# Optimization experiments

Hardware: AMD Instinct MI355X
Metric: run time of the kernel (lower is better)

## Reference

```python
import jax, jax.numpy as jnp
import numpy as np
import math

N_STATIONS = 50  # N in [N, 7, 56] causal matrix


def setup_inputs() -> dict:
    key = jax.random.key(0)
    k1, k2, k3, k4 = jax.random.split(key, 4)
    B, L, H, E = 3200, 7, 8, 64
    S, D = 56, 64
    queries = jax.random.normal(k1, (B, L, H, E), dtype=jnp.float32)
    keys = jax.random.normal(k2, (B, S, H, E), dtype=jnp.float32)
    values = jax.random.normal(k3, (B, S, H, D), dtype=jnp.float32)
    # station-specific multiplicative causal matrix in [0, 1]
    attn_mask = jax.random.uniform(k4, (N_STATIONS, L, S), dtype=jnp.float32)
    return {"queries": queries, "keys": keys, "values": values, "attn_mask": attn_mask}


def reference(queries, keys, values, attn_mask):
    B, L, H, E = queries.shape
    S = values.shape[1]
    N = attn_mask.shape[0]  # number of stations; B % N == 0
    ab = B // N  # actual batch size per station group
    scale = 1.0 / math.sqrt(E)
    # raw scores [B, H, L, S]
    scores = jnp.einsum('blhe,bshe->bhls', queries, keys)
    # multiplicative station-specific mask: reshape batch into (ab, N) and
    # broadcast mask [N, L, S] over (ab, H)
    masked = scores.reshape(ab, N, H, L, S) * attn_mask[None, :, None, :, :]
    masked = masked.reshape(B, H, L, S)
    # note: scale is applied AFTER masking, as in the original module
    A = jax.nn.softmax(scale * masked, axis=-1)  # dropout is identity at eval
    V = jnp.einsum('bhls,bshd->blhd', A, values)
    return V
```

## Files before the change

kernel.cpp:

```cpp
#include <hip/hip_runtime.h>
#include <math.h>


typedef __attribute__((ext_vector_type(8))) _Float16 half8;

#define GLDS(gp, lp) __builtin_amdgcn_global_load_lds(                        \
    (const __attribute__((address_space(1))) void*)(gp),                      \
    (__attribute__((address_space(3))) void*)(lp), 16, 0, 0)

__launch_bounds__(64, 4)
__global__ void fullattn_kernel(const float* __restrict__ q,
                                const float* __restrict__ k,
                                const float* __restrict__ v,
                                const float* __restrict__ mask,
                                float* __restrict__ out,
                                int nstations) {
    __shared__ __align__(16) float    KL[56 * 64];
    __shared__ __align__(16) float    VL[56 * 64];
    __shared__ __align__(16) _Float16 QL[7 * 64];

    const int lane = threadIdx.x;
    const int unit = blockIdx.x;
    const int b    = unit >> 3;
    const int h    = unit & 7;
    const int st   = b % nstations;

    const int kbase = b * 28672 + h * 64;
    const int qbase = b * 3584  + h * 64;

    {
        const int r = (lane >> 4);
        const int p = lane & 15;
#pragma unroll
        for (int j = 0; j < 14; ++j) {
            const int row = j * 4 + r;
            const int c   = p ^ (row & 15);
            GLDS(k + kbase + row * 512 + c * 4, (char*)KL + j * 1024);
        }
    }
    __builtin_amdgcn_sched_barrier(0);

    float qr[7];
#pragma unroll
    for (int l = 0; l < 7; ++l) qr[l] = q[qbase + l * 512 + lane];
    __builtin_amdgcn_sched_barrier(0);

    const int ml = (lane < 56) ? lane : 55;
    float m[7];
#pragma unroll
    for (int l = 0; l < 7; ++l)
        m[l] = mask[st * 392 + l * 56 + ml] * 0.125f;
    __builtin_amdgcn_sched_barrier(0);

    {
        const int r = (lane >> 4);
        const int p = lane & 15;
#pragma unroll
        for (int j = 0; j < 14; ++j) {
            const int row = j * 4 + r;
            GLDS(v + kbase + row * 512 + p * 4, (char*)VL + j * 1024);
        }
    }
    __builtin_amdgcn_sched_barrier(0);

    asm volatile("s_waitcnt vmcnt(28)" ::: "memory");
    __builtin_amdgcn_sched_barrier(0);

#pragma unroll
    for (int l = 0; l < 7; ++l) QL[l * 64 + lane] = (_Float16)qr[l];

    const int x16 = ml & 15;
    float acc[7];
#pragma unroll
    for (int l = 0; l < 7; ++l) acc[l] = 0.0f;

#pragma unroll
    for (int c2 = 0; c2 < 8; ++c2) {
        const float4 kv0 = *(const float4*)(&KL[ml * 64 + (((2 * c2)     ^ x16) << 2)]);
        const float4 kv1 = *(const float4*)(&KL[ml * 64 + (((2 * c2 + 1) ^ x16) << 2)]);
#pragma unroll
        for (int l = 0; l < 7; ++l) {
            const half8 qv = *(const half8*)(&QL[l * 64 + c2 * 8]);
            acc[l] = fmaf(kv0.x, (float)qv[0], acc[l]);
            acc[l] = fmaf(kv0.y, (float)qv[1], acc[l]);
            acc[l] = fmaf(kv0.z, (float)qv[2], acc[l]);
            acc[l] = fmaf(kv0.w, (float)qv[3], acc[l]);
            acc[l] = fmaf(kv1.x, (float)qv[4], acc[l]);
            acc[l] = fmaf(kv1.y, (float)qv[5], acc[l]);
            acc[l] = fmaf(kv1.z, (float)qv[6], acc[l]);
            acc[l] = fmaf(kv1.w, (float)qv[7], acc[l]);
        }
    }

    float* pbuf = (float*)KL;
    float rdenom[7];
#pragma unroll
    for (int l = 0; l < 7; ++l) {
        const float sc = acc[l] * m[l];
        const float p  = (lane < 56) ? __expf(sc) : 0.0f;
        float sum = p;
#pragma unroll
        for (int off = 32; off >= 1; off >>= 1)
            sum += __shfl_xor(sum, off);
        pbuf[l * 64 + lane] = p;
        rdenom[l] = __builtin_amdgcn_rcpf(sum);
    }

    asm volatile("s_waitcnt vmcnt(0)" ::: "memory");
    __builtin_amdgcn_sched_barrier(0);

    float facc[7];
#pragma unroll
    for (int l = 0; l < 7; ++l) facc[l] = 0.0f;

#pragma unroll
    for (int s4 = 0; s4 < 14; ++s4) {
        const float vv0 = VL[(s4 * 4 + 0) * 64 + lane];
        const float vv1 = VL[(s4 * 4 + 1) * 64 + lane];
        const float vv2 = VL[(s4 * 4 + 2) * 64 + lane];
        const float vv3 = VL[(s4 * 4 + 3) * 64 + lane];
#pragma unroll
        for (int l = 0; l < 7; ++l) {
            const float4 p4 = *(const float4*)(&pbuf[l * 64 + s4 * 4]);
            facc[l] = fmaf(p4.x, vv0, facc[l]);
            facc[l] = fmaf(p4.y, vv1, facc[l]);
            facc[l] = fmaf(p4.z, vv2, facc[l]);
            facc[l] = fmaf(p4.w, vv3, facc[l]);
        }
    }

#pragma unroll
    for (int l = 0; l < 7; ++l)
        out[qbase + l * 512 + lane] = facc[l] * rdenom[l];
}

extern "C" void kernel_launch(void* const* d_in, const int* in_sizes, int n_in,
                              void* d_out, int out_size, void* d_ws, size_t ws_size,
                              hipStream_t stream) {
    const float* q    = (const float*)d_in[0];
    const float* k    = (const float*)d_in[1];
    const float* v    = (const float*)d_in[2];
    const float* mask = (const float*)d_in[3];
    float* out        = (float*)d_out;

    const int B = in_sizes[0] / (7 * 8 * 64);
    const int nstations = in_sizes[3] / (7 * 56);

    fullattn_kernel<<<dim3(B * 8), dim3(64), 0, stream>>>(q, k, v, mask, out, nstations);
}
```

Before: 160.6 us.

## Convert to persistent kernel with double-buffered K/V prefetch across units

Replaces the one-block-per-(batch, head) launch with 512 persistent single-wave blocks. Each block loops over a contiguous range of units and double-buffers K/V in LDS. While one unit computes, the next unit's K/V (async global-to-LDS) and its Q and mask values are already being fetched, with hand-tuned vmcnt waits between stages. This aims to hide load latency and block launch overhead, but it lowers resident waves per CU and relies on exact vmcnt accounting.

```diff
diff --git a/kernel.cpp b/kernel.cpp
--- a/kernel.cpp
+++ b/kernel.cpp
@@ -8,130 +8,154 @@
     (const __attribute__((address_space(1))) void*)(gp),                      \
     (__attribute__((address_space(3))) void*)(lp), 16, 0, 0)
 
-__launch_bounds__(64, 4)
+__launch_bounds__(64, 1)
 __global__ void fullattn_kernel(const float* __restrict__ q,
                                 const float* __restrict__ k,
                                 const float* __restrict__ v,
                                 const float* __restrict__ mask,
                                 float* __restrict__ out,
-                                int nstations) {
-    __shared__ __align__(16) float    KL[56 * 64];
-    __shared__ __align__(16) float    VL[56 * 64];
+                                int nstations, int nunits, int nblocks) {
+    __shared__ __align__(16) float K0[56 * 64];
+    __shared__ __align__(16) float K1[56 * 64];
+    __shared__ __align__(16) float V0[56 * 64];
+    __shared__ __align__(16) float V1[56 * 64];
     __shared__ __align__(16) _Float16 QL[7 * 64];
 
     const int lane = threadIdx.x;
-    const int unit = blockIdx.x;
-    const int b    = unit >> 3;
-    const int h    = unit & 7;
-    const int st   = b % nstations;
+    const int bid  = blockIdx.x;
+    const int ustart = (int)(((long long)bid * nunits) / nblocks);
+    const int uend   = (int)(((long long)(bid + 1) * nunits) / nblocks);
+    if (ustart >= uend) return;
 
-    const int kbase = b * 28672 + h * 64;
-    const int qbase = b * 3584  + h * 64;
+    const int ml = (lane < 56) ? lane : 55;
+    const int rr = lane >> 4;
+    const int pp = lane & 15;
 
-    {
-        const int r = (lane >> 4);
-        const int p = lane & 15;
+    float qr_a[7], m_a[7], qr_b[7], m_b[7];
+
+    auto issue_kv = [&](int u, float* KB, float* VB) {
+        const int kbase = (u >> 3) * 28672 + (u & 7) * 64;
 #pragma unroll
         for (int j = 0; j < 14; ++j) {
-            const int row = j * 4 + r;
-            const int c   = p ^ (row & 15);
-            GLDS(k + kbase + row * 512 + c * 4, (char*)KL + j * 1024);
+            const int row = j * 4 + rr;
+            const int c   = pp ^ (row & 15);
+            GLDS(k + kbase + row * 512 + c * 4, (char*)KB + j * 1024);
         }
-    }
-    __builtin_amdgcn_sched_barrier(0);
-
-    float qr[7];
-#pragma unroll
-    for (int l = 0; l < 7; ++l) qr[l] = q[qbase + l * 512 + lane];
-    __builtin_amdgcn_sched_barrier(0);
-
-    const int ml = (lane < 56) ? lane : 55;
-    float m[7];
-#pragma unroll
-    for (int l = 0; l < 7; ++l)
-        m[l] = mask[st * 392 + l * 56 + ml] * 0.125f;
-    __builtin_amdgcn_sched_barrier(0);
-
-    {
-        const int r = (lane >> 4);
-        const int p = lane & 15;
 #pragma unroll
         for (int j = 0; j < 14; ++j) {
-            const int row = j * 4 + r;
-            GLDS(v + kbase + row * 512 + p * 4, (char*)VL + j * 1024);
+            const int row = j * 4 + rr;
+            GLDS(v + kbase + row * 512 + pp * 4, (char*)VB + j * 1024);
         }
-    }
-    __builtin_amdgcn_sched_barrier(0);
+    };
+    auto load_qm = [&](int u, float (&qr)[7], float (&m)[7]) {
+        const int qbase = (u >> 3) * 3584 + (u & 7) * 64;
+#pragma unroll
+        for (int l = 0; l < 7; ++l) qr[l] = q[qbase + l * 512 + lane];
+        const int st = (u >> 3) % nstations;
+#pragma unroll
+        for (int l = 0; l < 7; ++l)
+            m[l] = mask[st * 392 + l * 56 + ml] * 0.125f;
+    };
+    auto compute = [&](int u, float* KB, float* VB,
+                       const float (&qr)[7], const float (&m)[7]) {
+#pragma unroll
+        for (int l = 0; l < 7; ++l) QL[l * 64 + lane] = (_Float16)qr[l];
 
-    asm volatile("s_waitcnt vmcnt(28)" ::: "memory");
-    __builtin_amdgcn_sched_barrier(0);
+        const int x16 = ml & 15;
+        float acc[7];
+#pragma unroll
+        for (int l = 0; l < 7; ++l) acc[l] = 0.0f;
 
 #pragma unroll
-    for (int l = 0; l < 7; ++l) QL[l * 64 + lane] = (_Float16)qr[l];
+        for (int c2 = 0; c2 < 8; ++c2) {
+            const float4 kv0 = *(const float4*)(&KB[ml * 64 + (((2 * c2)     ^ x16) << 2)]);
+            const float4 kv1 = *(const float4*)(&KB[ml * 64 + (((2 * c2 + 1) ^ x16) << 2)]);
+#pragma unroll
+            for (int l = 0; l < 7; ++l) {
+                const half8 qv = *(const half8*)(&QL[l * 64 + c2 * 8]);
+                acc[l] = fmaf(kv0.x, (float)qv[0], acc[l]);
+                acc[l] = fmaf(kv0.y, (float)qv[1], acc[l]);
+                acc[l] = fmaf(kv0.z, (float)qv[2], acc[l]);
+                acc[l] = fmaf(kv0.w, (float)qv[3], acc[l]);
+                acc[l] = fmaf(kv1.x, (float)qv[4], acc[l]);
+                acc[l] = fmaf(kv1.y, (float)qv[5], acc[l]);
+                acc[l] = fmaf(kv1.z, (float)qv[6], acc[l]);
+                acc[l] = fmaf(kv1.w, (float)qv[7], acc[l]);
+            }
+        }
 
-    const int x16 = ml & 15;
-    float acc[7];
-#pragma unroll
-    for (int l = 0; l < 7; ++l) acc[l] = 0.0f;
-
-#pragma unroll
-    for (int c2 = 0; c2 < 8; ++c2) {
-        const float4 kv0 = *(const float4*)(&KL[ml * 64 + (((2 * c2)     ^ x16) << 2)]);
-        const float4 kv1 = *(const float4*)(&KL[ml * 64 + (((2 * c2 + 1) ^ x16) << 2)]);
+        float* pbuf = KB;
+        float rdenom[7];
 #pragma unroll
         for (int l = 0; l < 7; ++l) {
-            const half8 qv = *(const half8*)(&QL[l * 64 + c2 * 8]);
-            acc[l] = fmaf(kv0.x, (float)qv[0], acc[l]);
-            acc[l] = fmaf(kv0.y, (float)qv[1], acc[l]);
-            acc[l] = fmaf(kv0.z, (float)qv[2], acc[l]);
-            acc[l] = fmaf(kv0.w, (float)qv[3], acc[l]);
-            acc[l] = fmaf(kv1.x, (float)qv[4], acc[l]);
-            acc[l] = fmaf(kv1.y, (float)qv[5], acc[l]);
-            acc[l] = fmaf(kv1.z, (float)qv[6], acc[l]);
-            acc[l] = fmaf(kv1.w, (float)qv[7], acc[l]);
+            const float sc = acc[l] * m[l];
+            const float p  = (lane < 56) ? __expf(sc) : 0.0f;
+            float sum = p;
+#pragma unroll
+            for (int off = 32; off >= 1; off >>= 1)
+                sum += __shfl_xor(sum, off);
+            pbuf[l * 64 + lane] = p;
+            rdenom[l] = __builtin_amdgcn_rcpf(sum);
         }
+
+        float facc[7];
+#pragma unroll
+        for (int l = 0; l < 7; ++l) facc[l] = 0.0f;
+#pragma unroll
+        for (int s4 = 0; s4 < 14; ++s4) {
+            const float vv0 = VB[(s4 * 4 + 0) * 64 + lane];
+            const float vv1 = VB[(s4 * 4 + 1) * 64 + lane];
+            const float vv2 = VB[(s4 * 4 + 2) * 64 + lane];
+            const float vv3 = VB[(s4 * 4 + 3) * 64 + lane];
+#pragma unroll
+            for (int l = 0; l < 7; ++l) {
+                const float4 p4 = *(const float4*)(&pbuf[l * 64 + s4 * 4]);
+                facc[l] = fmaf(p4.x, vv0, facc[l]);
+                facc[l] = fmaf(p4.y, vv1, facc[l]);
+                facc[l] = fmaf(p4.z, vv2, facc[l]);
+                facc[l] = fmaf(p4.w, vv3, facc[l]);
+            }
+        }
+
+        const int qbase = (u >> 3) * 3584 + (u & 7) * 64;
+#pragma unroll
+        for (int l = 0; l < 7; ++l)
+            out[qbase + l * 512 + lane] = facc[l] * rdenom[l];
+    };
+
+    auto main_iter = [&](int u, float* KR, float* VR, float* KW, float* VW,
+                         const float (&qc)[7], const float (&mc)[7],
+                         float (&qn)[7], float (&mn)[7]) {
+        issue_kv(u + 1, KW, VW);
+        load_qm(u + 1, qn, mn);
+        __builtin_amdgcn_sched_barrier(0);
+        asm volatile("s_waitcnt vmcnt(49)" ::: "memory");
+        __builtin_amdgcn_sched_barrier(0);
+        compute(u, KR, VR, qc, mc);
+    };
+    auto last_iter = [&](int u, float* KR, float* VR,
+                         const float (&qc)[7], const float (&mc)[7]) {
+        __builtin_amdgcn_sched_barrier(0);
+        asm volatile("s_waitcnt vmcnt(7)" ::: "memory");
+        __builtin_amdgcn_sched_barrier(0);
+        compute(u, KR, VR, qc, mc);
+    };
+
+    issue_kv(ustart, K0, V0);
+    load_qm(ustart, qr_a, m_a);
+
+    int u = ustart;
+    while (u + 2 < uend) {
+        main_iter(u,     K0, V0, K1, V1, qr_a, m_a, qr_b, m_b);
+        main_iter(u + 1, K1, V1, K0, V0, qr_b, m_b, qr_a, m_a);
+        u += 2;
     }
-
-    float* pbuf = (float*)KL;
-    float rdenom[7];
-#pragma unroll
-    for (int l = 0; l < 7; ++l) {
-        const float sc = acc[l] * m[l];
-        const float p  = (lane < 56) ? __expf(sc) : 0.0f;
-        float sum = p;
-#pragma unroll
-        for (int off = 32; off >= 1; off >>= 1)
-            sum += __shfl_xor(sum, off);
-        pbuf[l * 64 + lane] = p;
-        rdenom[l] = __builtin_amdgcn_rcpf(sum);
+    if (u + 1 < uend) {
+        main_iter(u, K0, V0, K1, V1, qr_a, m_a, qr_b, m_b);
+        last_iter(u + 1, K1, V1, qr_b, m_b);
+    } else {
+        last_iter(u, K0, V0, qr_a, m_a);
     }
-
-    asm volatile("s_waitcnt vmcnt(0)" ::: "memory");
-    __builtin_amdgcn_sched_barrier(0);
-
-    float facc[7];
-#pragma unroll
-    for (int l = 0; l < 7; ++l) facc[l] = 0.0f;
-
-#pragma unroll
-    for (int s4 = 0; s4 < 14; ++s4) {
-        const float vv0 = VL[(s4 * 4 + 0) * 64 + lane];
-        const float vv1 = VL[(s4 * 4 + 1) * 64 + lane];
-        const float vv2 = VL[(s4 * 4 + 2) * 64 + lane];
-        const float vv3 = VL[(s4 * 4 + 3) * 64 + lane];
-#pragma unroll
-        for (int l = 0; l < 7; ++l) {
-            const float4 p4 = *(const float4*)(&pbuf[l * 64 + s4 * 4]);
-            facc[l] = fmaf(p4.x, vv0, facc[l]);
-            facc[l] = fmaf(p4.y, vv1, facc[l]);
-            facc[l] = fmaf(p4.z, vv2, facc[l]);
-            facc[l] = fmaf(p4.w, vv3, facc[l]);
-        }
-    }
-
-#pragma unroll
-    for (int l = 0; l < 7; ++l)
-        out[qbase + l * 512 + lane] = facc[l] * rdenom[l];
 }
 
 extern "C" void kernel_launch(void* const* d_in, const int* in_sizes, int n_in,
@@ -145,6 +169,9 @@
 
     const int B = in_sizes[0] / (7 * 8 * 64);
     const int nstations = in_sizes[3] / (7 * 56);
+    const int nunits = B * 8;
+    const int nblocks = 512;
 
-    fullattn_kernel<<<dim3(B * 8), dim3(64), 0, stream>>>(q, k, v, mask, out, nstations);
+    fullattn_kernel<<<dim3(nblocks), dim3(64), 0, stream>>>(q, k, v, mask, out,
+                                                            nstations, nunits, nblocks);
 }
```

Measured after the change: 262.2 us. 63.3% more time.

## Use MFMA f16 matrix instructions for QK^T and PV in attention kernel

Applied to the files above, without the earlier changes.

Replaces the scalar FMA loops for both score computation and the P·V product with 16x16x32 f16 MFMA instructions. K is converted to a swizzled f16 LDS copy, Q and probabilities are staged in padded f16 LDS tiles, and the softmax reduction now runs over the MFMA output layout. The waitcnt and launch bounds change to fit the new load order and higher register use. This adds LDS traffic for the conversions and wastes MFMA work on padding rows (7 of 16 used), which lowers occupancy and may cost accuracy.

```diff
diff --git a/kernel.cpp b/kernel.cpp
--- a/kernel.cpp
+++ b/kernel.cpp
@@ -3,12 +3,14 @@
 
 
 typedef __attribute__((ext_vector_type(8))) _Float16 half8;
+typedef __attribute__((ext_vector_type(4))) _Float16 half4;
+typedef __attribute__((ext_vector_type(4))) float floatx4;
 
 #define GLDS(gp, lp) __builtin_amdgcn_global_load_lds(                        \
     (const __attribute__((address_space(1))) void*)(gp),                      \
     (__attribute__((address_space(3))) void*)(lp), 16, 0, 0)
 
-__launch_bounds__(64, 4)
+__launch_bounds__(64, 2)
 __global__ void fullattn_kernel(const float* __restrict__ q,
                                 const float* __restrict__ k,
                                 const float* __restrict__ v,
@@ -17,7 +19,9 @@
                                 int nstations) {
     __shared__ __align__(16) float    KL[56 * 64];
     __shared__ __align__(16) float    VL[56 * 64];
-    __shared__ __align__(16) _Float16 QL[7 * 64];
+    __shared__ __align__(16) _Float16 K16[56 * 64];
+    __shared__ __align__(16) _Float16 Q16[7 * 64];
+    __shared__ __align__(16) _Float16 P16[16 * 64];
 
     const int lane = threadIdx.x;
     const int unit = blockIdx.x;
@@ -28,15 +32,14 @@
     const int kbase = b * 28672 + h * 64;
     const int qbase = b * 3584  + h * 64;
 
-    {
-        const int r = (lane >> 4);
-        const int p = lane & 15;
+    const int rr  = lane >> 4;
+    const int col = lane & 15;
+
 #pragma unroll
-        for (int j = 0; j < 14; ++j) {
-            const int row = j * 4 + r;
-            const int c   = p ^ (row & 15);
-            GLDS(k + kbase + row * 512 + c * 4, (char*)KL + j * 1024);
-        }
+    for (int j = 0; j < 14; ++j) {
+        const int row  = j * 4 + rr;
+        const int csrc = col ^ (row & 15);
+        GLDS(k + kbase + row * 512 + csrc * 4, (char*)KL + j * 1024);
     }
     __builtin_amdgcn_sched_barrier(0);
 
@@ -45,93 +48,106 @@
     for (int l = 0; l < 7; ++l) qr[l] = q[qbase + l * 512 + lane];
     __builtin_amdgcn_sched_barrier(0);
 
-    const int ml = (lane < 56) ? lane : 55;
-    float m[7];
+    float mm[4][4];
 #pragma unroll
-    for (int l = 0; l < 7; ++l)
-        m[l] = mask[st * 392 + l * 56 + ml] * 0.125f;
+    for (int nt = 0; nt < 4; ++nt)
+#pragma unroll
+        for (int reg = 0; reg < 4; ++reg) {
+            const int mrow = (rr * 4 + reg < 7) ? (rr * 4 + reg) : 6;
+            const int mcol = (col + 16 * nt < 56) ? (col + 16 * nt) : 55;
+            mm[nt][reg] = mask[st * 392 + mrow * 56 + mcol] * 0.125f;
+        }
     __builtin_amdgcn_sched_barrier(0);
 
-    {
-        const int r = (lane >> 4);
-        const int p = lane & 15;
 #pragma unroll
-        for (int j = 0; j < 14; ++j) {
-            const int row = j * 4 + r;
-            GLDS(v + kbase + row * 512 + p * 4, (char*)VL + j * 1024);
-        }
+    for (int j = 0; j < 14; ++j) {
+        const int row = j * 4 + rr;
+        GLDS(v + kbase + row * 512 + col * 4, (char*)VL + j * 1024);
     }
     __builtin_amdgcn_sched_barrier(0);
 
-    asm volatile("s_waitcnt vmcnt(28)" ::: "memory");
+    asm volatile("s_waitcnt vmcnt(30)" ::: "memory");
     __builtin_amdgcn_sched_barrier(0);
 
 #pragma unroll
-    for (int l = 0; l < 7; ++l) QL[l * 64 + lane] = (_Float16)qr[l];
-
-    const int x16 = ml & 15;
-    float acc[7];
-#pragma unroll
-    for (int l = 0; l < 7; ++l) acc[l] = 0.0f;
+    for (int l = 0; l < 7; ++l)
+        Q16[l * 64 + (lane ^ ((l & 7) << 3))] = (_Float16)qr[l];
 
 #pragma unroll
-    for (int c2 = 0; c2 < 8; ++c2) {
-        const float4 kv0 = *(const float4*)(&KL[ml * 64 + (((2 * c2)     ^ x16) << 2)]);
-        const float4 kv1 = *(const float4*)(&KL[ml * 64 + (((2 * c2 + 1) ^ x16) << 2)]);
+    for (int i = 0; i < 14; ++i) {
+        const int f  = i * 64 + lane;
+        const int s  = f >> 4;
+        const int lc = f & 15;
+        const floatx4 a = *(const floatx4*)(&KL[s * 64 + ((lc ^ (s & 15)) << 2)]);
+        half4 hv;
+        hv[0] = (_Float16)a[0]; hv[1] = (_Float16)a[1];
+        hv[2] = (_Float16)a[2]; hv[3] = (_Float16)a[3];
+        *(half4*)(&K16[s * 64 + ((lc << 2) ^ ((s & 7) << 3))]) = hv;
+    }
+
+    floatx4 acc[4] = {{0.f,0.f,0.f,0.f},{0.f,0.f,0.f,0.f},
+                      {0.f,0.f,0.f,0.f},{0.f,0.f,0.f,0.f}};
+    const int qrow = (col < 7) ? col : 0;
 #pragma unroll
-        for (int l = 0; l < 7; ++l) {
-            const half8 qv = *(const half8*)(&QL[l * 64 + c2 * 8]);
-            acc[l] = fmaf(kv0.x, (float)qv[0], acc[l]);
-            acc[l] = fmaf(kv0.y, (float)qv[1], acc[l]);
-            acc[l] = fmaf(kv0.z, (float)qv[2], acc[l]);
-            acc[l] = fmaf(kv0.w, (float)qv[3], acc[l]);
-            acc[l] = fmaf(kv1.x, (float)qv[4], acc[l]);
-            acc[l] = fmaf(kv1.y, (float)qv[5], acc[l]);
-            acc[l] = fmaf(kv1.z, (float)qv[6], acc[l]);
-            acc[l] = fmaf(kv1.w, (float)qv[7], acc[l]);
+    for (int kc = 0; kc < 2; ++kc) {
+        const int koff = kc * 32 + rr * 8;
+        const half8 af = *(const half8*)(&Q16[qrow * 64 + (koff ^ ((qrow & 7) << 3))]);
+#pragma unroll
+        for (int nt = 0; nt < 4; ++nt) {
+            const int sr = (col + 16 * nt < 56) ? (col + 16 * nt) : 55;
+            const half8 bf = *(const half8*)(&K16[sr * 64 + (koff ^ ((sr & 7) << 3))]);
+            acc[nt] = __builtin_amdgcn_mfma_f32_16x16x32_f16(af, bf, acc[nt], 0, 0, 0);
         }
     }
 
-    float* pbuf = (float*)KL;
-    float rdenom[7];
+    float rden[4];
 #pragma unroll
-    for (int l = 0; l < 7; ++l) {
-        const float sc = acc[l] * m[l];
-        const float p  = (lane < 56) ? __expf(sc) : 0.0f;
-        float sum = p;
+    for (int reg = 0; reg < 4; ++reg) {
+        float s_r = 0.0f;
+        const int prow = rr * 4 + reg;
 #pragma unroll
-        for (int off = 32; off >= 1; off >>= 1)
-            sum += __shfl_xor(sum, off);
-        pbuf[l * 64 + lane] = p;
-        rdenom[l] = __builtin_amdgcn_rcpf(sum);
+        for (int nt = 0; nt < 4; ++nt) {
+            const float sc = acc[nt][reg] * mm[nt][reg];
+            float p = __expf(sc);
+            if (nt == 3 && (lane & 8)) p = 0.0f;
+            P16[prow * 64 + ((col + 16 * nt) ^ ((prow & 7) << 3))] = (_Float16)p;
+            s_r += p;
+        }
+#pragma unroll
+        for (int off = 1; off <= 8; off <<= 1)
+            s_r += __shfl_xor(s_r, off);
+        rden[reg] = __builtin_amdgcn_rcpf(s_r);
     }
 
     asm volatile("s_waitcnt vmcnt(0)" ::: "memory");
     __builtin_amdgcn_sched_barrier(0);
 
-    float facc[7];
+    floatx4 facc[4] = {{0.f,0.f,0.f,0.f},{0.f,0.f,0.f,0.f},
+                       {0.f,0.f,0.f,0.f},{0.f,0.f,0.f,0.f}};
 #pragma unroll
-    for (int l = 0; l < 7; ++l) facc[l] = 0.0f;
-
+    for (int kc = 0; kc < 2; ++kc) {
+        const int koff = kc * 32 + rr * 8;
+        const half8 paf = *(const half8*)(&P16[col * 64 + (koff ^ ((col & 7) << 3))]);
 #pragma unroll
-    for (int s4 = 0; s4 < 14; ++s4) {
-        const float vv0 = VL[(s4 * 4 + 0) * 64 + lane];
-        const float vv1 = VL[(s4 * 4 + 1) * 64 + lane];
-        const float vv2 = VL[(s4 * 4 + 2) * 64 + lane];
-        const float vv3 = VL[(s4 * 4 + 3) * 64 + lane];
+        for (int nt = 0; nt < 4; ++nt) {
+            half8 vbf;
 #pragma unroll
-        for (int l = 0; l < 7; ++l) {
-            const float4 p4 = *(const float4*)(&pbuf[l * 64 + s4 * 4]);
-            facc[l] = fmaf(p4.x, vv0, facc[l]);
-            facc[l] = fmaf(p4.y, vv1, facc[l]);
-            facc[l] = fmaf(p4.z, vv2, facc[l]);
-            facc[l] = fmaf(p4.w, vv3, facc[l]);
+            for (int jj = 0; jj < 8; ++jj) {
+                const int sidx = (koff + jj < 56) ? (koff + jj) : 55;
+                vbf[jj] = (_Float16)VL[sidx * 64 + col + 16 * nt];
+            }
+            facc[nt] = __builtin_amdgcn_mfma_f32_16x16x32_f16(paf, vbf, facc[nt], 0, 0, 0);
         }
     }
 
 #pragma unroll
-    for (int l = 0; l < 7; ++l)
-        out[qbase + l * 512 + lane] = facc[l] * rdenom[l];
+    for (int nt = 0; nt < 4; ++nt)
+#pragma unroll
+        for (int reg = 0; reg < 4; ++reg) {
+            const int orow = rr * 4 + reg;
+            if (orow < 7)
+                out[qbase + orow * 512 + col + 16 * nt] = facc[nt][reg] * rden[reg];
+        }
 }
 
 extern "C" void kernel_launch(void* const* d_in, const int* in_sizes, int n_in,
```

New measurement: 162.1 us. About the same (+0.9%).
